# Kernel tuning notes

Hardware: AMD Instinct MI355X
Metric: run time of the kernel (lower is better)

## Reference

```python
import jax, jax.numpy as jnp
import numpy as np

N, E = 50000, 800000          # nodes, edges
H, C = 4, 64                  # heads, out_channels
F_IN, F_E = 5, 1              # node feature dim, edge feature dim
NEG_SLOPE = 0.2               # PyG GATConv default LeakyReLU slope
EPS = 1e-16                   # PyG softmax denominator epsilon


def setup_inputs() -> dict:
    key = jax.random.key(0)
    ks = jax.random.split(key, 10)
    return {
        "x": jax.random.normal(ks[0], (N, F_IN), jnp.float32),
        "edge_attr": jax.random.normal(ks[1], (E, F_E), jnp.float32),
        "u": jax.random.normal(ks[2], (1, 1), jnp.float32),
        # learned params (glorot-ish scale)
        "W": jax.random.normal(ks[3], (F_IN, H * C), jnp.float32) * 0.3,
        "W_edge": jax.random.normal(ks[4], (F_E, H * C), jnp.float32) * 0.3,
        "att_src": jax.random.normal(ks[5], (H, C), jnp.float32) * 0.1,
        "att_dst": jax.random.normal(ks[6], (H, C), jnp.float32) * 0.1,
        "att_edge": jax.random.normal(ks[7], (H, C), jnp.float32) * 0.1,
        "bias": jnp.zeros((C,), jnp.float32),
        "edge_index": jax.random.randint(ks[8], (2, E), 0, N, dtype=jnp.int32),
        "batch": jnp.zeros((N,), jnp.int32),
    }


def reference(x, edge_attr, u, W, W_edge, att_src, att_dst, att_edge, bias,
              edge_index, batch):
    # dropout p=0.0 is identity; u and batch are unused by the module's forward.
    src, dst = edge_index[0], edge_index[1]

    # node transform: [N, H, C]
    h = (x @ W).reshape(-1, H, C)
    # per-node attention logits: [N, H]
    a_src = jnp.einsum("nhc,hc->nh", h, att_src)
    a_dst = jnp.einsum("nhc,hc->nh", h, att_dst)

    # edge transform + edge attention logits: [E, H]
    e = (edge_attr @ W_edge).reshape(-1, H, C)
    a_edge = jnp.einsum("ehc,hc->eh", e, att_edge)

    # per-edge logits, LeakyReLU: [E, H]
    alpha = jax.nn.leaky_relu(a_src[src] + a_dst[dst] + a_edge, NEG_SLOPE)

    # segment softmax grouped by destination node
    m = jax.ops.segment_max(alpha, dst, num_segments=N)        # [N, H]
    alpha = jnp.exp(alpha - m[dst])
    s = jax.ops.segment_sum(alpha, dst, num_segments=N)        # [N, H]
    alpha = alpha / (s[dst] + EPS)

    # weighted scatter-aggregate of source features: [N, H, C]
    msg = h[src] * alpha[:, :, None]                           # [E, H, C]
    out = jax.ops.segment_sum(msg, dst, num_segments=N)

    # concat=False -> mean over heads, then bias: [N, C]
    return out.mean(axis=1) + bias
```

## Files before the change

### kernel.cpp

```cpp
#include <hip/hip_runtime.h>
#include <hip/hip_fp16.h>

#define N_NODES 50000
#define N_EDGES 800000
#define NH 4
#define NC 64
#define HC 256
#define F_IN 5
#define NEG_SLOPE 0.2f
#define SM_EPS 1e-16f
#define CAP 64
#define EPT 4
#define NPB 64
#define NODE_CHUNKS ((N_NODES + 255) / 256)
#define PLACE_GRID ((N_EDGES + 256 * EPT - 1) / (256 * EPT))
#define GO_GRID ((N_NODES + NPB - 1) / NPB)

__device__ __forceinline__ float wave_reduce_sum(float v) {
#pragma unroll
    for (int o = 32; o > 0; o >>= 1) v += __shfl_xor(v, o, 64);
    return v;
}

__global__ __launch_bounds__(256) void nodeprep_kernel(
        const float* __restrict__ x, const float* __restrict__ W,
        const float* __restrict__ att_src, const float* __restrict__ att_dst,
        float4* __restrict__ a_src4, float4* __restrict__ a_dst4,
        float* __restrict__ xp, int* __restrict__ cursor) {
    __shared__ float Vs[F_IN][NH], Vd[F_IN][NH];
    const int t = threadIdx.x;
    const int head = t >> 6, lane = t & 63;
    const float asv = att_src[t], adv = att_dst[t];
#pragma unroll
    for (int f = 0; f < F_IN; ++f) {
        const float w = W[f * HC + t];
        float vs = wave_reduce_sum(w * asv);
        float vd = wave_reduce_sum(w * adv);
        if (lane == 0) { Vs[f][head] = vs; Vd[f][head] = vd; }
    }
    __syncthreads();

    const int n = blockIdx.x * 256 + t;
    if (n >= N_NODES) return;
    float xs[F_IN];
#pragma unroll
    for (int f = 0; f < F_IN; ++f) xs[f] = x[n * F_IN + f];
    float as[NH] = {0.f, 0.f, 0.f, 0.f}, ad[NH] = {0.f, 0.f, 0.f, 0.f};
#pragma unroll
    for (int f = 0; f < F_IN; ++f)
#pragma unroll
        for (int h = 0; h < NH; ++h) {
            as[h] += xs[f] * Vs[f][h];
            ad[h] += xs[f] * Vd[f][h];
        }
    a_src4[n] = make_float4(as[0], as[1], as[2], as[3]);
    a_dst4[n] = make_float4(ad[0], ad[1], ad[2], ad[3]);
    float* xpn = xp + (size_t)n * 8;
    ((float4*)xpn)[0] = make_float4(xs[0], xs[1], xs[2], xs[3]);
    ((float4*)xpn)[1] = make_float4(xs[4], 0.f, 0.f, 0.f);
    cursor[n] = 0;
}

__global__ __launch_bounds__(256) void place_kernel(
        const int* __restrict__ ei, const float* __restrict__ edge_attr,
        int* __restrict__ cursor, unsigned int* __restrict__ rec) {
    const int e0 = (blockIdx.x * 256 + threadIdx.x) * EPT;
    if (e0 >= N_EDGES) return;
    if (e0 + EPT <= N_EDGES) {
        const int4 s4 = *(const int4*)(ei + e0);
        const int4 d4 = *(const int4*)(ei + N_EDGES + e0);
        const float4 a4 = *(const float4*)(edge_attr + e0);
        const int ss[EPT] = {s4.x, s4.y, s4.z, s4.w};
        const int dd[EPT] = {d4.x, d4.y, d4.z, d4.w};
        const float aa[EPT] = {a4.x, a4.y, a4.z, a4.w};
        int slot[EPT];
#pragma unroll
        for (int k = 0; k < EPT; ++k) slot[k] = atomicAdd(&cursor[dd[k]], 1);
#pragma unroll
        for (int k = 0; k < EPT; ++k) {
            if (slot[k] < CAP) {
                const unsigned int h16 =
                    (unsigned int)__half_as_ushort(__float2half(aa[k]));
                rec[(size_t)dd[k] * CAP + slot[k]] =
                    ((unsigned int)ss[k] << 16) | h16;
            }
        }
    } else {
        for (int e = e0; e < N_EDGES; ++e) {
            const int src = ei[e];
            const int dst = ei[N_EDGES + e];
            const int slot = atomicAdd(&cursor[dst], 1);
            if (slot < CAP) {
                const unsigned int h16 =
                    (unsigned int)__half_as_ushort(__float2half(edge_attr[e]));
                rec[(size_t)dst * CAP + slot] = ((unsigned int)src << 16) | h16;
            }
        }
    }
}

__global__ __launch_bounds__(256) void gatherout_kernel(
        const float* __restrict__ W_edge, const float* __restrict__ att_edge,
        const int* __restrict__ cursor, const unsigned int* __restrict__ rec,
        const float4* __restrict__ a_src4, const float4* __restrict__ a_dst4,
        const float* __restrict__ xp, const float* __restrict__ W,
        const float* __restrict__ bias, float* __restrict__ out) {
    __shared__ float aeS[NH];
    __shared__ float nacc[NPB][21];
    const int t = threadIdx.x;
    {
        const int head = t >> 6, lane = t & 63;
        float v = wave_reduce_sum(W_edge[t] * att_edge[t]);
        if (lane == 0) aeS[head] = v;
    }
    __syncthreads();
    const float ae0 = aeS[0], ae1 = aeS[1], ae2 = aeS[2], ae3 = aeS[3];

    const int nl = t >> 2, parity = t & 3;
    const int n = blockIdx.x * NPB + nl;

    float acc[NH][F_IN];
#pragma unroll
    for (int h = 0; h < NH; ++h)
#pragma unroll
        for (int f = 0; f < F_IN; ++f) acc[h][f] = 0.f;
    float sden[NH] = {0.f, 0.f, 0.f, 0.f};

    if (n < N_NODES) {
        int cnt = cursor[n];
        cnt = cnt < CAP ? cnt : CAP;
        const float4 ad = a_dst4[n];
        const unsigned int* rp = rec + (size_t)n * CAP;
        for (int i = parity; i < cnt; i += 4) {
            const unsigned int r = rp[i];
            const int src = (int)(r >> 16);
            const float ea = __half2float(__ushort_as_half((unsigned short)(r & 0xffffu)));
            const float4 as = a_src4[src];
            float l0 = as.x + ad.x + ea * ae0;
            float l1 = as.y + ad.y + ea * ae1;
            float l2 = as.z + ad.z + ea * ae2;
            float l3 = as.w + ad.w + ea * ae3;
            l0 = l0 > 0.f ? l0 : NEG_SLOPE * l0;
            l1 = l1 > 0.f ? l1 : NEG_SLOPE * l1;
            l2 = l2 > 0.f ? l2 : NEG_SLOPE * l2;
            l3 = l3 > 0.f ? l3 : NEG_SLOPE * l3;
            const float p0 = expf(l0), p1 = expf(l1), p2 = expf(l2), p3 = expf(l3);
            const float* xr = xp + (size_t)src * 8;
            const float4 xa = *(const float4*)xr;
            const float x4v = xr[4];
            const float xs[F_IN] = {xa.x, xa.y, xa.z, xa.w, x4v};
            const float pv[NH] = {p0, p1, p2, p3};
#pragma unroll
            for (int h = 0; h < NH; ++h) {
                sden[h] += pv[h];
#pragma unroll
                for (int f = 0; f < F_IN; ++f) acc[h][f] += pv[h] * xs[f];
            }
        }
    }
#pragma unroll
    for (int h = 0; h < NH; ++h) {
        sden[h] += __shfl_xor(sden[h], 1, 64);
        sden[h] += __shfl_xor(sden[h], 2, 64);
#pragma unroll
        for (int f = 0; f < F_IN; ++f) {
            acc[h][f] += __shfl_xor(acc[h][f], 1, 64);
            acc[h][f] += __shfl_xor(acc[h][f], 2, 64);
        }
    }
    if (parity == 0 && n < N_NODES) {
#pragma unroll
        for (int h = 0; h < NH; ++h) {
            const float is = 0.25f / (sden[h] + SM_EPS);
#pragma unroll
            for (int f = 0; f < F_IN; ++f) nacc[nl][h * F_IN + f] = acc[h][f] * is;
        }
    }
    __syncthreads();

    const int c = t & 63;
    float wreg[NH][F_IN];
#pragma unroll
    for (int h = 0; h < NH; ++h)
#pragma unroll
        for (int f = 0; f < F_IN; ++f) wreg[h][f] = W[f * HC + h * NC + c];
    const float bv = bias[c];
#pragma unroll
    for (int k = 0; k < NPB / 4; ++k) {
        const int nl2 = k * 4 + (t >> 6);
        const int n2 = blockIdx.x * NPB + nl2;
        if (n2 < N_NODES) {
            float r = bv;
#pragma unroll
            for (int h = 0; h < NH; ++h)
#pragma unroll
                for (int f = 0; f < F_IN; ++f)
                    r += nacc[nl2][h * F_IN + f] * wreg[h][f];
            out[(size_t)n2 * NC + c] = r;
        }
    }
}

extern "C" void kernel_launch(void* const* d_in, const int* in_sizes, int n_in,
                              void* d_out, int out_size, void* d_ws, size_t ws_size,
                              hipStream_t stream) {
    const float* x         = (const float*)d_in[0];
    const float* edge_attr = (const float*)d_in[1];
    const float* W         = (const float*)d_in[3];
    const float* W_edge    = (const float*)d_in[4];
    const float* att_src   = (const float*)d_in[5];
    const float* att_dst   = (const float*)d_in[6];
    const float* att_edge  = (const float*)d_in[7];
    const float* bias      = (const float*)d_in[8];
    const int*   ei        = (const int*)d_in[9];
    float* out = (float*)d_out;

    float* f = (float*)d_ws;
    size_t off = 0;
    float* a_src = f + off; off += (size_t)N_NODES * 4;
    float* a_dst = f + off; off += (size_t)N_NODES * 4;
    float* xp    = f + off; off += (size_t)N_NODES * 8;
    int* cursor  = (int*)(f + off); off += N_NODES;
    unsigned int* rec = (unsigned int*)(f + off);

    nodeprep_kernel<<<NODE_CHUNKS, 256, 0, stream>>>(x, W, att_src, att_dst,
                                                     (float4*)a_src, (float4*)a_dst,
                                                     xp, cursor);
    place_kernel<<<PLACE_GRID, 256, 0, stream>>>(ei, edge_attr, cursor, rec);
    gatherout_kernel<<<GO_GRID, 256, 0, stream>>>(W_edge, att_edge, cursor, rec,
                                                  (const float4*)a_src,
                                                  (const float4*)a_dst, xp, W,
                                                  bias, out);
}
```

Measured before the change: 155.5 us.

## Merge node prep and edge placement into one launch; pack per-node record

The node-prep and edge-placement kernels are merged into a single launch that splits work by block index. The cursor reset moves to a memset so the two halves no longer depend on each other. Per-node a_src, x and a_dst are packed into one 64-byte record, so the gather reads the source's logits and features from a single cache line instead of two arrays. This trades one extra memset for one fewer kernel launch, and the wider record adds padding bytes to the node data.

Measured after the change: 149.0 us. 1.04x faster.

```diff
diff --git a/kernel.cpp b/kernel.cpp
--- a/kernel.cpp
+++ b/kernel.cpp
@@ -12,8 +12,8 @@
 #define CAP 64
 #define EPT 4
 #define NPB 64
-#define NODE_CHUNKS ((N_NODES + 255) / 256)
-#define PLACE_GRID ((N_EDGES + 256 * EPT - 1) / (256 * EPT))
+#define PREP_BLOCKS ((N_NODES + 255) / 256)
+#define PLACE_BLOCKS ((N_EDGES + 256 * EPT - 1) / (256 * EPT))
 #define GO_GRID ((N_NODES + NPB - 1) / NPB)
 
 __device__ __forceinline__ float wave_reduce_sum(float v) {
@@ -22,78 +22,77 @@
     return v;
 }
 
-__global__ __launch_bounds__(256) void nodeprep_kernel(
+__global__ __launch_bounds__(256) void prep_place_kernel(
         const float* __restrict__ x, const float* __restrict__ W,
         const float* __restrict__ att_src, const float* __restrict__ att_dst,
-        float4* __restrict__ a_src4, float4* __restrict__ a_dst4,
-        float* __restrict__ xp, int* __restrict__ cursor) {
-    __shared__ float Vs[F_IN][NH], Vd[F_IN][NH];
+        const int* __restrict__ ei, const float* __restrict__ edge_attr,
+        float* __restrict__ nrec, int* __restrict__ cursor,
+        unsigned int* __restrict__ rec) {
     const int t = threadIdx.x;
-    const int head = t >> 6, lane = t & 63;
-    const float asv = att_src[t], adv = att_dst[t];
-#pragma unroll
-    for (int f = 0; f < F_IN; ++f) {
-        const float w = W[f * HC + t];
-        float vs = wave_reduce_sum(w * asv);
-        float vd = wave_reduce_sum(w * adv);
-        if (lane == 0) { Vs[f][head] = vs; Vd[f][head] = vd; }
-    }
-    __syncthreads();
-
-    const int n = blockIdx.x * 256 + t;
-    if (n >= N_NODES) return;
-    float xs[F_IN];
-#pragma unroll
-    for (int f = 0; f < F_IN; ++f) xs[f] = x[n * F_IN + f];
-    float as[NH] = {0.f, 0.f, 0.f, 0.f}, ad[NH] = {0.f, 0.f, 0.f, 0.f};
-#pragma unroll
-    for (int f = 0; f < F_IN; ++f)
-#pragma unroll
-        for (int h = 0; h < NH; ++h) {
-            as[h] += xs[f] * Vs[f][h];
-            ad[h] += xs[f] * Vd[f][h];
-        }
-    a_src4[n] = make_float4(as[0], as[1], as[2], as[3]);
-    a_dst4[n] = make_float4(ad[0], ad[1], ad[2], ad[3]);
-    float* xpn = xp + (size_t)n * 8;
-    ((float4*)xpn)[0] = make_float4(xs[0], xs[1], xs[2], xs[3]);
-    ((float4*)xpn)[1] = make_float4(xs[4], 0.f, 0.f, 0.f);
-    cursor[n] = 0;
-}
-
-__global__ __launch_bounds__(256) void place_kernel(
-        const int* __restrict__ ei, const float* __restrict__ edge_attr,
-        int* __restrict__ cursor, unsigned int* __restrict__ rec) {
-    const int e0 = (blockIdx.x * 256 + threadIdx.x) * EPT;
-    if (e0 >= N_EDGES) return;
-    if (e0 + EPT <= N_EDGES) {
-        const int4 s4 = *(const int4*)(ei + e0);
-        const int4 d4 = *(const int4*)(ei + N_EDGES + e0);
-        const float4 a4 = *(const float4*)(edge_attr + e0);
-        const int ss[EPT] = {s4.x, s4.y, s4.z, s4.w};
-        const int dd[EPT] = {d4.x, d4.y, d4.z, d4.w};
-        const float aa[EPT] = {a4.x, a4.y, a4.z, a4.w};
-        int slot[EPT];
-#pragma unroll
-        for (int k = 0; k < EPT; ++k) slot[k] = atomicAdd(&cursor[dd[k]], 1);
-#pragma unroll
-        for (int k = 0; k < EPT; ++k) {
-            if (slot[k] < CAP) {
-                const unsigned int h16 =
-                    (unsigned int)__half_as_ushort(__float2half(aa[k]));
-                rec[(size_t)dd[k] * CAP + slot[k]] =
-                    ((unsigned int)ss[k] << 16) | h16;
-            }
-        }
+    if (blockIdx.x < PREP_BLOCKS) {
+        __shared__ float Vs[F_IN][NH], Vd[F_IN][NH];
+        const int head = t >> 6, lane = t & 63;
+        const float asv = att_src[t], adv = att_dst[t];
+#pragma unroll
+        for (int f = 0; f < F_IN; ++f) {
+            const float w = W[f * HC + t];
+            float vs = wave_reduce_sum(w * asv);
+            float vd = wave_reduce_sum(w * adv);
+            if (lane == 0) { Vs[f][head] = vs; Vd[f][head] = vd; }
+        }
+        __syncthreads();
+
+        const int n = blockIdx.x * 256 + t;
+        if (n >= N_NODES) return;
+        float xs[F_IN];
+#pragma unroll
+        for (int f = 0; f < F_IN; ++f) xs[f] = x[n * F_IN + f];
+        float as[NH] = {0.f, 0.f, 0.f, 0.f}, ad[NH] = {0.f, 0.f, 0.f, 0.f};
+#pragma unroll
+        for (int f = 0; f < F_IN; ++f)
+#pragma unroll
+            for (int h = 0; h < NH; ++h) {
+                as[h] += xs[f] * Vs[f][h];
+                ad[h] += xs[f] * Vd[f][h];
+            }
+        float* r = nrec + (size_t)n * 16;
+        ((float4*)r)[0] = make_float4(as[0], as[1], as[2], as[3]);
+        ((float4*)r)[1] = make_float4(xs[0], xs[1], xs[2], xs[3]);
+        ((float4*)r)[2] = make_float4(xs[4], 0.f, 0.f, 0.f);
+        ((float4*)r)[3] = make_float4(ad[0], ad[1], ad[2], ad[3]);
     } else {
-        for (int e = e0; e < N_EDGES; ++e) {
-            const int src = ei[e];
-            const int dst = ei[N_EDGES + e];
-            const int slot = atomicAdd(&cursor[dst], 1);
-            if (slot < CAP) {
-                const unsigned int h16 =
-                    (unsigned int)__half_as_ushort(__float2half(edge_attr[e]));
-                rec[(size_t)dst * CAP + slot] = ((unsigned int)src << 16) | h16;
+        const int pb = blockIdx.x - PREP_BLOCKS;
+        const int e0 = (pb * 256 + t) * EPT;
+        if (e0 >= N_EDGES) return;
+        if (e0 + EPT <= N_EDGES) {
+            const int4 s4 = *(const int4*)(ei + e0);
+            const int4 d4 = *(const int4*)(ei + N_EDGES + e0);
+            const float4 a4 = *(const float4*)(edge_attr + e0);
+            const int ss[EPT] = {s4.x, s4.y, s4.z, s4.w};
+            const int dd[EPT] = {d4.x, d4.y, d4.z, d4.w};
+            const float aa[EPT] = {a4.x, a4.y, a4.z, a4.w};
+            int slot[EPT];
+#pragma unroll
+            for (int k = 0; k < EPT; ++k) slot[k] = atomicAdd(&cursor[dd[k]], 1);
+#pragma unroll
+            for (int k = 0; k < EPT; ++k) {
+                if (slot[k] < CAP) {
+                    const unsigned int h16 =
+                        (unsigned int)__half_as_ushort(__float2half(aa[k]));
+                    rec[(size_t)dd[k] * CAP + slot[k]] =
+                        ((unsigned int)ss[k] << 16) | h16;
+                }
+            }
+        } else {
+            for (int e = e0; e < N_EDGES; ++e) {
+                const int src = ei[e];
+                const int dst = ei[N_EDGES + e];
+                const int slot = atomicAdd(&cursor[dst], 1);
+                if (slot < CAP) {
+                    const unsigned int h16 =
+                        (unsigned int)__half_as_ushort(__float2half(edge_attr[e]));
+                    rec[(size_t)dst * CAP + slot] = ((unsigned int)src << 16) | h16;
+                }
             }
         }
     }
@@ -102,8 +101,7 @@
 __global__ __launch_bounds__(256) void gatherout_kernel(
         const float* __restrict__ W_edge, const float* __restrict__ att_edge,
         const int* __restrict__ cursor, const unsigned int* __restrict__ rec,
-        const float4* __restrict__ a_src4, const float4* __restrict__ a_dst4,
-        const float* __restrict__ xp, const float* __restrict__ W,
+        const float* __restrict__ nrec, const float* __restrict__ W,
         const float* __restrict__ bias, float* __restrict__ out) {
     __shared__ float aeS[NH];
     __shared__ float nacc[NPB][21];
@@ -129,13 +127,16 @@
     if (n < N_NODES) {
         int cnt = cursor[n];
         cnt = cnt < CAP ? cnt : CAP;
-        const float4 ad = a_dst4[n];
+        const float4 ad = ((const float4*)(nrec + (size_t)n * 16))[3];
         const unsigned int* rp = rec + (size_t)n * CAP;
         for (int i = parity; i < cnt; i += 4) {
             const unsigned int r = rp[i];
             const int src = (int)(r >> 16);
             const float ea = __half2float(__ushort_as_half((unsigned short)(r & 0xffffu)));
-            const float4 as = a_src4[src];
+            const float* sr = nrec + (size_t)src * 16;
+            const float4 as = ((const float4*)sr)[0];
+            const float4 xa = ((const float4*)sr)[1];
+            const float x4v = sr[8];
             float l0 = as.x + ad.x + ea * ae0;
             float l1 = as.y + ad.y + ea * ae1;
             float l2 = as.z + ad.z + ea * ae2;
@@ -145,9 +146,6 @@
             l2 = l2 > 0.f ? l2 : NEG_SLOPE * l2;
             l3 = l3 > 0.f ? l3 : NEG_SLOPE * l3;
             const float p0 = expf(l0), p1 = expf(l1), p2 = expf(l2), p3 = expf(l3);
-            const float* xr = xp + (size_t)src * 8;
-            const float4 xa = *(const float4*)xr;
-            const float x4v = xr[4];
             const float xs[F_IN] = {xa.x, xa.y, xa.z, xa.w, x4v};
             const float pv[NH] = {p0, p1, p2, p3};
 #pragma unroll
@@ -217,18 +215,13 @@
 
     float* f = (float*)d_ws;
     size_t off = 0;
-    float* a_src = f + off; off += (size_t)N_NODES * 4;
-    float* a_dst = f + off; off += (size_t)N_NODES * 4;
-    float* xp    = f + off; off += (size_t)N_NODES * 8;
+    float* nrec  = f + off; off += (size_t)N_NODES * 16;
     int* cursor  = (int*)(f + off); off += N_NODES;
     unsigned int* rec = (unsigned int*)(f + off);
 
-    nodeprep_kernel<<<NODE_CHUNKS, 256, 0, stream>>>(x, W, att_src, att_dst,
-                                                     (float4*)a_src, (float4*)a_dst,
-                                                     xp, cursor);
-    place_kernel<<<PLACE_GRID, 256, 0, stream>>>(ei, edge_attr, cursor, rec);
+    hipMemsetAsync(cursor, 0, N_NODES * sizeof(int), stream);
+    prep_place_kernel<<<PREP_BLOCKS + PLACE_BLOCKS, 256, 0, stream>>>(
+        x, W, att_src, att_dst, ei, edge_attr, nrec, cursor, rec);
     gatherout_kernel<<<GO_GRID, 256, 0, stream>>>(W_edge, att_edge, cursor, rec,
-                                                  (const float4*)a_src,
-                                                  (const float4*)a_dst, xp, W,
-                                                  bias, out);
-}
+                                                  nrec, W, bias, out);
+}
```
